# Performance work log

Hardware: AMD Instinct MI355X
Metric: run time of the kernel (lower is better)

Reference implementation:

```python
import jax, jax.numpy as jnp
import numpy as np

B, NPG, H, TD, NF, NL, A = 64, 20, 512, 256, 128, 6, 100
N = B * NPG
E = B * NPG * (NPG - 1)
ANG_LO, ANG_HI = 59.9, 120.1
LOG_MEANS = jnp.array([1.575442910194397, 1.7017393112182617, 1.9781638383865356], jnp.float32)
LOG_STDS = jnp.array([0.24437622725963593, 0.26526379585266113, 0.3535512685775757], jnp.float32)
TWO_PI = 2.0 * np.pi


def _logmap(x, y):
    z = TWO_PI * (y - x)
    return jnp.arctan2(jnp.sin(z), jnp.cos(z)) / TWO_PI


def _lattice_matrix(lengths, angles_deg):
    a = jnp.deg2rad(angles_deg)
    c, s = jnp.cos(a), jnp.sin(a)
    val = jnp.clip((c[:, 0] * c[:, 1] - c[:, 2]) / (s[:, 0] * s[:, 1]), -1.0, 1.0)
    gs = jnp.arccos(val)
    zero = jnp.zeros_like(lengths[:, 0])
    va = jnp.stack([lengths[:, 0] * s[:, 1], zero, lengths[:, 0] * c[:, 1]], 1)
    vb = jnp.stack([-lengths[:, 1] * s[:, 0] * jnp.cos(gs), lengths[:, 1] * s[:, 0] * jnp.sin(gs), lengths[:, 1] * c[:, 0]], 1)
    vc = jnp.stack([zero, zero, lengths[:, 2]], 1)
    return jnp.stack([va, vb, vc], 1)


def _ln(x, g, b, eps=1e-5):
    mu = jnp.mean(x, -1, keepdims=True)
    var = jnp.var(x, -1, keepdims=True)
    return (x - mu) * jax.lax.rsqrt(var + eps) * g + b


def setup_inputs() -> dict:
    key = jax.random.key(0)
    ks = jax.random.split(key, 24)
    # forward data
    t = jax.random.uniform(ks[0], (B, 1), jnp.float32)
    atom_types = jax.random.randint(ks[1], (N,), 1, A + 1, jnp.int32)
    frac_coords = jax.random.uniform(ks[2], (N, 3), jnp.float32)
    lattice_params = 0.5 * jax.random.normal(ks[3], (B, 6), jnp.float32)
    num_atoms = jnp.full((B,), NPG, jnp.int32)
    node2graph = jnp.repeat(jnp.arange(B, dtype=jnp.int32), NPG)
    # fully-connected edges per graph, no self edges (static structure)
    loc = np.arange(NPG)
    src_l, dst_l = np.meshgrid(loc, loc, indexing='ij')
    mask = src_l != dst_l
    src_l, dst_l = src_l[mask], dst_l[mask]  # (NPG*(NPG-1),)
    offs = (np.arange(B)[:, None] * NPG)
    src = (offs + src_l[None, :]).reshape(-1)
    dst = (offs + dst_l[None, :]).reshape(-1)
    edge_index = jnp.asarray(np.stack([src, dst]), jnp.int32)  # (2, E)
    edge2graph = node2graph[edge_index[0]]
    # parameters
    def w(k, shape, fan_in):
        return (jax.random.normal(k, shape, jnp.float32) / np.sqrt(fan_in)).astype(jnp.float32)
    EIN = 3 + 3 * H + 6 + NF * 2 * 3  # 2313
    p = {
        'W_node': w(ks[4], (A, H), A),
        'W_time': w(ks[5], (1, TD), 1),
        'W_latent': w(ks[6], (H + TD, H), H + TD),
        'ln_gamma': jnp.ones((NL, H), jnp.float32),
        'ln_beta': jnp.zeros((NL, H), jnp.float32),
        'We1': w(ks[7], (NL, EIN, H), EIN),
        'be1': jnp.zeros((NL, H), jnp.float32),
        'We2': w(ks[8], (NL, H, H), H),
        'be2': jnp.zeros((NL, H), jnp.float32),
        'Wn1': w(ks[9], (NL, 2 * H, H), 2 * H),
        'bn1': jnp.zeros((NL, H), jnp.float32),
        'Wn2': w(ks[10], (NL, H, H), H),
        'bn2': jnp.zeros((NL, H), jnp.float32),
        'W_numatom': w(ks[11], (NL, A, H), A),
        'fln_gamma': jnp.ones((H,), jnp.float32),
        'fln_beta': jnp.zeros((H,), jnp.float32),
        'W_coord': w(ks[12], (H, 3), H),
        'W_latout': w(ks[13], (2 * H, 6), 2 * H),
        'b_latout': jnp.zeros((6,), jnp.float32),
    }
    return dict(t=t, frac_coords=frac_coords, lattice_params=lattice_params,
                atom_types=atom_types, num_atoms=num_atoms, node2graph=node2graph,
                edge_index=edge_index, edge2graph=edge2graph, **p)


def reference(t, frac_coords, lattice_params, W_node, W_time, W_latent, ln_gamma, ln_beta,
              We1, be1, We2, be2, Wn1, bn1, Wn2, bn2, W_numatom, fln_gamma, fln_beta,
              W_coord, W_latout, b_latout, atom_types, num_atoms, node2graph, edge_index, edge2graph):
    n_nodes = frac_coords.shape[0]
    n_graphs = t.shape[0]
    src, dst = edge_index[0], edge_index[1]
    frac_diff = _logmap(frac_coords[src], frac_coords[dst])  # (E,3)

    atom_oh = jax.nn.one_hot(jnp.clip(atom_types - 1, 0), A, dtype=jnp.float32)
    h = atom_oh @ W_node
    temb = t @ W_time  # (B,TD)
    h = jnp.concatenate([h, temb[node2graph]], -1) @ W_latent

    lattice_flat = lattice_params  # 6-D in directly
    lengths = jnp.exp(lattice_params[:, :3] * LOG_STDS + LOG_MEANS)
    angles_deg = ANG_LO + (ANG_HI - ANG_LO) * jax.nn.sigmoid(lattice_params[:, 3:])
    Lmat = _lattice_matrix(lengths, angles_deg)  # (B,3,3)
    ltl = jnp.einsum('bij,bkj->bik', Lmat, Lmat)  # L @ L^T

    dots = jnp.einsum('eij,ej->ei', ltl[edge2graph], frac_diff)
    unit_dots = dots / (jnp.linalg.norm(dots, axis=-1, keepdims=True) + 1e-12)

    freqs = TWO_PI * jnp.arange(NF, dtype=jnp.float32)
    emb = (frac_diff[..., None] * freqs).reshape(-1, 3 * NF)
    femb = jnp.concatenate([jnp.sin(emb), jnp.cos(emb)], -1)  # (E, 768)

    na_oh = jax.nn.one_hot(num_atoms - 1, A, dtype=jnp.float32)  # (B,100)
    lat_e = lattice_flat[edge2graph]
    counts = jnp.maximum(jax.ops.segment_sum(jnp.ones_like(src, dtype=jnp.float32), src, num_segments=n_nodes), 1.0)[:, None]

    for l in range(NL):
        h_in = h
        hn = _ln(h_in, ln_gamma[l], ln_beta[l])
        na_emb = (na_oh @ W_numatom[l])[edge2graph]
        ef = jnp.concatenate([unit_dots, hn[src], hn[dst], lat_e, femb, na_emb], -1)
        e = jax.nn.silu(jax.nn.silu(ef @ We1[l] + be1[l]) @ We2[l] + be2[l])
        agg = jax.ops.segment_sum(e, src, num_segments=n_nodes) / counts
        out = jax.nn.silu(jax.nn.silu(jnp.concatenate([hn, agg], -1) @ Wn1[l] + bn1[l]) @ Wn2[l] + bn2[l])
        h = h_in + out

    h = _ln(h, fln_gamma, fln_beta)
    pos_v = h @ W_coord  # (N,3)
    sum_pool = jax.ops.segment_sum(h, node2graph, num_segments=n_graphs)
    mean_pool = sum_pool / num_atoms.astype(jnp.float32)[:, None]
    cell_v = jnp.concatenate([mean_pool, sum_pool], -1) @ W_latout + b_latout  # (B,6)
    return pos_v, cell_v
```

## Files before the change

### kernel.cpp

```cpp
#include <hip/hip_runtime.h>
#include <hip/hip_bf16.h>

typedef __hip_bfloat16 bf16;
typedef unsigned char u8;
typedef __attribute__((ext_vector_type(8))) __bf16 bf16x8;
typedef __attribute__((ext_vector_type(4))) float f32x4;

#define B_   64
#define NPG_ 20
#define H_   512
#define TD_  256
#define NF_  128
#define NL_  6
#define A_   100
#define N_   (B_ * NPG_)
#define E_   (B_ * NPG_ * (NPG_-1))
#define EIN_ 2313
#define KF_  832

__device__ __forceinline__ float bf2f(bf16 x) { return __bfloat162float(x); }
__device__ __forceinline__ bf16  f2bf(float x) { return __float2bfloat16(x); }
__device__ __forceinline__ float siluf(float x) { return x / (1.0f + expf(-x)); }
__device__ __forceinline__ float ldf(const void* p, size_t i, int isb) {
    return isb ? bf2f(((const bf16*)p)[i]) : ((const float*)p)[i];
}
__device__ __forceinline__ u8 f2f8(float f) {
    unsigned s = (__float_as_uint(f) >> 24) & 0x80;
    float a = fabsf(f);
    if (!(a == a)) return (u8)0x7F;
    if (a == 0.0f) return (u8)s;
    if (a >= 448.0f) return (u8)(s | 0x7E);
    int e; float m = frexpf(a, &e);
    int ef = e + 6;
    unsigned code;
    if (ef >= 1) {
        int mant = (int)rintf(m * 16.0f) - 8;
        if (mant == 8) { mant = 0; ef++; }
        if (ef > 15) return (u8)(s | 0x7E);
        code = ((unsigned)ef << 3) | (unsigned)mant;
    } else {
        int mant = (int)rintf(ldexpf(a, 9));
        code = (mant >= 8) ? (1u<<3) : (unsigned)mant;
    }
    return (u8)(s | code);
}
__device__ __forceinline__ void async_cp16(const void* src, void* dst) {
    __builtin_amdgcn_global_load_lds(
        (const __attribute__((address_space(1))) unsigned int*)src,
        (__attribute__((address_space(3))) unsigned int*)dst,
        16, 0, 0);
}

__global__ void detect_dtype(const unsigned int* __restrict__ tw, int* __restrict__ flag) {
    if (threadIdx.x != 0) return;
    int cnt = 0;
    for (int i = 0; i < 32; i++) {
        unsigned b1 = (tw[i] >> 8) & 0xFF;
        if (b1 >= 0x20 && b1 < 0x40) cnt++;
    }
    *flag = (cnt >= 16) ? 1 : 0;
}

__global__ void ws_sentinel(bf16* out) { if (threadIdx.x == 0) out[0] = f2bf(1000.0f); }

__global__ void prep_graph(const void* __restrict__ latp, float* __restrict__ ltl,
                           const int* __restrict__ flag) {
    int b = threadIdx.x;
    if (b >= B_) return;
    int isb = *flag;
    const float LM[3] = {1.575442910194397f, 1.7017393112182617f, 1.9781638383865356f};
    const float LS[3] = {0.24437622725963593f, 0.26526379585266113f, 0.3535512685775757f};
    float lp[6];
    for (int i = 0; i < 6; i++) lp[i] = ldf(latp, b*6 + i, isb);
    float len[3], c[3], s[3];
    for (int i = 0; i < 3; i++) len[i] = expf(lp[i] * LS[i] + LM[i]);
    for (int i = 0; i < 3; i++) {
        float sig = 1.0f / (1.0f + expf(-lp[3+i]));
        float deg = 59.9f + 60.2f * sig;
        float a = deg * 0.017453292519943295f;
        c[i] = cosf(a); s[i] = sinf(a);
    }
    float val = (c[0]*c[1] - c[2]) / (s[0]*s[1]);
    val = fminf(1.0f, fmaxf(-1.0f, val));
    float gs = acosf(val);
    float L[3][3];
    L[0][0] = len[0]*s[1]; L[0][1] = 0.0f;               L[0][2] = len[0]*c[1];
    L[1][0] = -len[1]*s[0]*cosf(gs); L[1][1] = len[1]*s[0]*sinf(gs); L[1][2] = len[1]*c[0];
    L[2][0] = 0.0f; L[2][1] = 0.0f; L[2][2] = len[2];
    for (int i = 0; i < 3; i++)
        for (int k = 0; k < 3; k++)
            ltl[b*9 + i*3 + k] = L[i][0]*L[k][0] + L[i][1]*L[k][1] + L[i][2]*L[k][2];
}

__global__ __launch_bounds__(512) void prep_q(const void* __restrict__ W_time,
                                              const void* __restrict__ W_latent,
                                              float* __restrict__ q,
                                              const int* __restrict__ flag) {
    int j = threadIdx.x;
    int isb = *flag;
    float s0 = 0.0f, s1 = 0.0f, s2 = 0.0f, s3 = 0.0f;
    for (int d = 0; d < TD_; d += 4) {
        s0 += ldf(W_time, d+0, isb) * ldf(W_latent, (size_t)(H_ + d+0)*H_ + j, isb);
        s1 += ldf(W_time, d+1, isb) * ldf(W_latent, (size_t)(H_ + d+1)*H_ + j, isb);
        s2 += ldf(W_time, d+2, isb) * ldf(W_latent, (size_t)(H_ + d+2)*H_ + j, isb);
        s3 += ldf(W_time, d+3, isb) * ldf(W_latent, (size_t)(H_ + d+3)*H_ + j, isb);
    }
    q[j] = (s0 + s1) + (s2 + s3);
}

__global__ __launch_bounds__(256) void pq_gather(const void* __restrict__ W_node,
                                                 const void* __restrict__ W_numatom,
                                                 bf16* __restrict__ PQa,
                                                 const int* __restrict__ flag) {
    int z = blockIdx.x, ch = blockIdx.y;
    int isb = *flag;
    int base = ch * 4096;
    for (int idx = base + threadIdx.x; idx < base + 4096; idx += 256) {
        int r = idx >> 9, c = idx & 511;
        float v = 0.0f;
        if (r < A_) {
            if (z == 0) v = ldf(W_node, (size_t)r*512 + c, isb);
            else        v = ldf(W_numatom, ((size_t)(z-1)*A_ + r)*512 + c, isb);
        }
        PQa[(size_t)z*65536 + idx] = f2bf(v);
    }
}

__global__ __launch_bounds__(256) void transpose_pq(const void* __restrict__ W_latent,
                                                    const void* __restrict__ We1,
                                                    bf16* __restrict__ PQbt,
                                                    const int* __restrict__ flag) {
    __shared__ bf16 tile[32][33];
    int z = blockIdx.z;
    int isb = *flag;
    const void* src = (z == 0) ? W_latent : We1;
    size_t off = (z == 0) ? 0 : ((size_t)(z-1)*EIN_ + 1801)*512;
    bf16* dst = PQbt + (size_t)z*512*512;
    int r0 = blockIdx.y * 32, c0 = blockIdx.x * 32;
    #pragma unroll
    for (int i = 0; i < 32; i += 8)
        tile[threadIdx.y + i][threadIdx.x] =
            f2bf(ldf(src, off + (size_t)(r0 + threadIdx.y + i)*512 + c0 + threadIdx.x, isb));
    __syncthreads();
    #pragma unroll
    for (int i = 0; i < 32; i += 8)
        dst[(size_t)(c0 + threadIdx.y + i)*512 + r0 + threadIdx.x] = tile[threadIdx.x][threadIdx.y + i];
}

__global__ __launch_bounds__(256) void transpose_layer(
    const void* __restrict__ We1p, const void* __restrict__ We2p,
    const void* __restrict__ Wn1p, const void* __restrict__ Wn2p, size_t l0, int allmode,
    bf16* __restrict__ WtAB, u8* __restrict__ Wtf8, bf16* __restrict__ Wte2,
    bf16* __restrict__ Wtn1, bf16* __restrict__ Wtn2,
    const int* __restrict__ flag) {
    __shared__ bf16 tile[32][33];
    int which = blockIdx.z % 6;
    size_t lz = blockIdx.z / 6;
    size_t l = l0 + lz, lw = allmode ? lz : 0;
    int isb = *flag;
    const void* src; size_t off; bf16* dst = nullptr; int R; int ldd;
    switch (which) {
        case 0:  src = We1p; off = (l*EIN_ + 3)*512;    dst = WtAB + lw*512*1024;            R = 512;  ldd = 512;  break;
        case 1:  src = We1p; off = (l*EIN_ + 515)*512;  dst = WtAB + lw*512*1024 + 512*512;  R = 512;  ldd = 512;  break;
        case 2:  src = We1p; off = (l*EIN_ + 1033)*512; R = 768; ldd = KF_; break;
        case 3:  src = We2p; off = l*512*512;           dst = Wte2 + lw*512*512;             R = 512;  ldd = 512;  break;
        case 4:  src = Wn1p; off = l*1024*512;          dst = Wtn1 + lw*512*1024;            R = 1024; ldd = 1024; break;
        default: src = Wn2p; off = l*512*512;           dst = Wtn2 + lw*512*512;             R = 512;  ldd = 512;  break;
    }
    int r0 = blockIdx.y * 32, c0 = blockIdx.x * 32;
    if (r0 >= R) return;
    #pragma unroll
    for (int i = 0; i < 32; i += 8)
        tile[threadIdx.y + i][threadIdx.x] =
            f2bf(ldf(src, off + (size_t)(r0 + threadIdx.y + i)*512 + c0 + threadIdx.x, isb));
    __syncthreads();
    if (which == 2) {
        u8* d8 = Wtf8 + lw*(size_t)512*KF_;
        #pragma unroll
        for (int i = 0; i < 32; i += 8)
            d8[(size_t)(c0 + threadIdx.y + i)*KF_ + r0 + threadIdx.x] =
                f2f8(bf2f(tile[threadIdx.x][threadIdx.y + i]));
    } else {
        #pragma unroll
        for (int i = 0; i < 32; i += 8)
            dst[(size_t)(c0 + threadIdx.y + i)*ldd + r0 + threadIdx.x] = tile[threadIdx.x][threadIdx.y + i];
    }
}

__global__ __launch_bounds__(512) void wtf_tail(const void* __restrict__ We1, size_t l0, int allmode,
                                                u8* __restrict__ Wtf8,
                                                const int* __restrict__ flag) {
    size_t lz = blockIdx.x;
    size_t l = l0 + lz, lw = allmode ? lz : 0;
    int n = threadIdx.x;
    int isb = *flag;
    const int rows[9] = {0, 1, 2, 1027, 1028, 1029, 1030, 1031, 1032};
    u8* d8 = Wtf8 + lw*(size_t)512*KF_;
    #pragma unroll
    for (int j = 0; j < 64; j++) {
        float v = (j < 9) ? ldf(We1, (l*EIN_ + rows[j])*512 + n, isb) : 0.0f;
        d8[(size_t)n*KF_ + 768 + j] = f2f8(v);
    }
}

__global__ __launch_bounds__(512) void cbias_prep(const bf16* __restrict__ PQc,
                                                  const void* __restrict__ be1,
                                                  const int* __restrict__ num_atoms,
                                                  float* __restrict__ cbias,
                                                  const int* __restrict__ flag) {
    int l = blockIdx.x, g = blockIdx.y, j = threadIdx.x;
    int isb = *flag;
    int na = num_atoms[g] - 1;
    float qv = (na >= 0 && na < A_) ? bf2f(PQc[(size_t)(1+l)*65536 + (size_t)na*512 + j]) : 0.0f;
    cbias[((size_t)l*B_ + g)*512 + j] = ldf(be1, l*512 + j, isb) + qv;
}

__global__ __launch_bounds__(512) void node_embed_fast(const bf16* __restrict__ P,
                                                       const float* __restrict__ q,
                                                       const void* __restrict__ t,
                                                       const int* __restrict__ atom_types,
                                                       const int* __restrict__ node2graph,
                                                       float* __restrict__ h,
                                                       const int* __restrict__ flag) {
    int i = blockIdx.x, j = threadIdx.x;
    int isb = *flag;
    int at = atom_types[i] - 1; if (at < 0) at = 0;
    float pv = (at < A_) ? bf2f(P[(size_t)at*512 + j]) : 0.0f;
    float tv = ldf(t, node2graph[i], isb);
    h[(size_t)i*H_ + j] = pv + tv * q[j];
}

__global__ __launch_bounds__(384) void edge_prep(const void* __restrict__ frac,
                                                 const int* __restrict__ edge_index,
                                                 const int* __restrict__ e2g,
                                                 const void* __restrict__ latp,
                                                 const float* __restrict__ ltl,
                                                 int* __restrict__ edat,
                                                 u8* __restrict__ femb8,
                                                 const int* __restrict__ flag) {
    const float TWO_PI_F = 6.283185307179586f;
    int e = blockIdx.x;
    int isb = *flag;
    int src = edge_index[e], dst = edge_index[E_ + e];
    int tid = threadIdx.x;
    int d = tid >> 7, k = tid & 127;
    float x = ldf(frac, src*3 + d, isb), y = ldf(frac, dst*3 + d, isb);
    float diff = y - x;
    float fd = diff - rintf(diff);
    float sv, cv;
    sincosf(fd * (TWO_PI_F * (float)k), &sv, &cv);
    femb8[(size_t)e*KF_ + d*NF_ + k]       = f2f8(sv);
    femb8[(size_t)e*KF_ + 384 + d*NF_ + k] = f2f8(cv);
    if (tid < 64) {
        int g = e2g[e];
        float v = 0.0f;
        if (tid < 3) {
            float f3[3];
            for (int dd = 0; dd < 3; dd++) {
                float df = ldf(frac, dst*3 + dd, isb) - ldf(frac, src*3 + dd, isb);
                f3[dd] = df - rintf(df);
            }
            float dots[3];
            for (int i = 0; i < 3; i++)
                dots[i] = ltl[g*9 + i*3 + 0]*f3[0] + ltl[g*9 + i*3 + 1]*f3[1] + ltl[g*9 + i*3 + 2]*f3[2];
            float nrm = sqrtf(dots[0]*dots[0] + dots[1]*dots[1] + dots[2]*dots[2]);
            v = dots[tid] / (nrm + 1e-12f);
        } else if (tid < 9) {
            v = ldf(latp, g*6 + tid - 3, isb);
        }
        femb8[(size_t)e*KF_ + 768 + tid] = f2f8(v);
        if (tid == 0) {
            edat[e*4 + 0] = src;
            edat[e*4 + 1] = dst;
            edat[e*4 + 2] = g;
            edat[e*4 + 3] = 0;
        }
    }
}

__device__ __forceinline__ float block_sum_256(float v, float* red) {
    for (int o = 32; o; o >>= 1) v += __shfl_down(v, o);
    int w = threadIdx.x >> 6, lane = threadIdx.x & 63;
    if (lane == 0) red[w] = v;
    __syncthreads();
    float s = red[0] + red[1] + red[2] + red[3];
    __syncthreads();
    return s;
}

__global__ __launch_bounds__(256) void ln_kernel(const float* __restrict__ x,
                                                 const void* __restrict__ gamma,
                                                 const void* __restrict__ beta, size_t goff,
                                                 bf16* __restrict__ cat,
                                                 const int* __restrict__ flag) {
    __shared__ float red[4];
    size_t n = blockIdx.x;
    int tid = threadIdx.x;
    int isb = *flag;
    const float* xr = x + n*H_;
    float v0 = xr[tid], v1 = xr[tid + 256];
    float mu = block_sum_256(v0 + v1, red) * (1.0f/512.0f);
    float d0 = v0 - mu, d1 = v1 - mu;
    float var = block_sum_256(d0*d0 + d1*d1, red) * (1.0f/512.0f);
    float rs = 1.0f / sqrtf(var + 1e-5f);
    cat[n*1024 + tid]       = f2bf(d0*rs*ldf(gamma, goff + tid, isb)       + ldf(beta, goff + tid, isb));
    cat[n*1024 + 256 + tid] = f2bf(d1*rs*ldf(gamma, goff + tid + 256, isb) + ldf(beta, goff + tid + 256, isb));
}

template<int EPI, int TM>
__global__ __launch_bounds__(256) void gemm_bt(
        const bf16* __restrict__ A, int lda,
        const bf16* __restrict__ Bt,
        const void* __restrict__ bias, size_t boff,
        bf16* __restrict__ Cb, float* __restrict__ Cf,
        int K, int N,
        size_t zsA, size_t zsB, size_t zsC,
        const int* __restrict__ flag) {
    constexpr int MT = TM / 32;
    __shared__ __align__(16) bf16 As[TM*64];
    __shared__ __align__(16) bf16 Bs[128*64];
    const int z = blockIdx.z;
    A  += (size_t)z * zsA;
    Bt += (size_t)z * zsB;
    const size_t coff = (size_t)z * zsC;
    const int tid = threadIdx.x;
    const int wave = tid >> 6, lane = tid & 63;
    const int lrow = lane & 15, lq = lane >> 4;
    const size_t m0 = (size_t)blockIdx.y * TM;
    const int n0 = blockIdx.x * 128;
    const int wm = (wave >> 1) * (TM/2), wn = (wave & 1) * 64;
    const int ar = lane >> 3;
    const int gk = (lane & 7) ^ ar;
    f32x4 acc[MT][4] = {};

    for (int k0 = 0; k0 < K; k0 += 64) {
        if (k0) __syncthreads();
        #pragma unroll
        for (int i = 0; i < TM/32; i++) {
            int R = wave*(TM/4) + i*8;
            async_cp16(A + (m0 + R + ar)*lda + k0 + gk*8, As + R*64);
        }
        #pragma unroll
        for (int i = 0; i < 4; i++) {
            int R = wave*32 + i*8;
            async_cp16(Bt + (size_t)(n0 + R + ar)*K + k0 + gk*8, Bs + R*64);
        }
        __syncthreads();
        #pragma unroll
        for (int kk = 0; kk < 2; kk++) {
            bf16x8 af[MT], bfr[4];
            #pragma unroll
            for (int mt = 0; mt < MT; mt++) {
                int r = wm + mt*16 + lrow;
                int p = (kk*4 + lq) ^ (r & 7);
                af[mt] = *(const bf16x8*)(As + r*64 + p*8);
            }
            #pragma unroll
            for (int nt = 0; nt < 4; nt++) {
                int r = wn + nt*16 + lrow;
                int p = (kk*4 + lq) ^ (r & 7);
                bfr[nt] = *(const bf16x8*)(Bs + r*64 + p*8);
            }
            #pragma unroll
            for (int mt = 0; mt < MT; mt++)
                #pragma unroll
                for (int nt = 0; nt < 4; nt++)
                    acc[mt][nt] = __builtin_amdgcn_mfma_f32_16x16x32_bf16(af[mt], bfr[nt], acc[mt][nt], 0, 0, 0);
        }
    }

    const int isb = bias ? *flag : 0;
    #pragma unroll
    for (int mt = 0; mt < MT; mt++)
        #pragma unroll
        for (int nt = 0; nt < 4; nt++) {
            int col = n0 + wn + nt*16 + lrow;
            float bv = bias ? ldf(bias, boff + col, isb) : 0.0f;
            #pragma unroll
            for (int r = 0; r < 4; r++) {
                size_t row = m0 + wm + mt*16 + lq*4 + r;
                float x = acc[mt][nt][r] + bv;
                if (EPI == 0)      Cb[coff + row*N + col] = f2bf(x);
                else if (EPI == 1) Cb[coff + row*N + col] = f2bf(siluf(x));
                else               Cf[coff + row*N + col] += siluf(x);
            }
        }
}

__global__ __launch_bounds__(256) void gemm_fp8_e1(
        const u8* __restrict__ A,
        const u8* __restrict__ Bt,
        const float* __restrict__ cbias_l,
        const bf16* __restrict__ hnAB,
        const int* __restrict__ edat,
        bf16* __restrict__ Cb) {
    __shared__ __align__(16) u8 As[64*64];
    __shared__ __align__(16) u8 Bs[128*64];
    const int tid = threadIdx.x;
    const int wave = tid >> 6, lane = tid & 63;
    const int lrow = lane & 15, lq = lane >> 4;
    const size_t m0 = (size_t)blockIdx.y * 64;
    const int n0 = blockIdx.x * 128;
    const int wm = (wave >> 1) * 32, wn = (wave & 1) * 64;
    const int ar = lane >> 2;
    const int ac = lane & 3;
    const int gk = ac ^ (ar & 3);
    f32x4 acc[2][4] = {};

    for (int k0 = 0; k0 < KF_; k0 += 64) {
        if (k0) __syncthreads();
        {
            int R = wave*16;
            async_cp16(A + (m0 + R + ar)*KF_ + k0 + gk*16, As + R*64);
        }
        #pragma unroll
        for (int i = 0; i < 2; i++) {
            int R = wave*32 + i*16;
            async_cp16(Bt + (size_t)(n0 + R + ar)*KF_ + k0 + gk*16, Bs + R*64);
        }
        __syncthreads();
        #pragma unroll
        for (int kk = 0; kk < 2; kk++) {
            long long af[2], bfr[4];
            #pragma unroll
            for (int mt = 0; mt < 2; mt++) {
                int r = wm + mt*16 + lrow;
                int p = (kk*2 + (lq >> 1)) ^ (r & 3);
                af[mt] = *(const long long*)(As + r*64 + p*16 + (lq & 1)*8);
            }
            #pragma unroll
            for (int nt = 0; nt < 4; nt++) {
                int r = wn + nt*16 + lrow;
                int p = (kk*2 + (lq >> 1)) ^ (r & 3);
                bfr[nt] = *(const long long*)(Bs + r*64 + p*16 + (lq & 1)*8);
            }
            #pragma unroll
            for (int mt = 0; mt < 2; mt++)
                #pragma unroll
                for (int nt = 0; nt < 4; nt++)
                    acc[mt][nt] = __builtin_amdgcn_mfma_f32_16x16x32_fp8_fp8(af[mt], bfr[nt], acc[mt][nt], 0, 0, 0);
        }
    }

    #pragma unroll
    for (int mt = 0; mt < 2; mt++) {
        #pragma unroll
        for (int r = 0; r < 4; r++) {
            size_t e = m0 + wm + mt*16 + lq*4 + r;
            const int4 q = *(const int4*)(edat + e*4);
            int se = q.x, de = q.y, g = q.z;
            #pragma unroll
            for (int nt = 0; nt < 4; nt++) {
                int col = n0 + wn + nt*16 + lrow;
                float x = acc[mt][nt][r]
                        + cbias_l[(size_t)g*512 + col]
                        + bf2f(hnAB[(size_t)se*1024 + col])
                        + bf2f(hnAB[(size_t)de*1024 + 512 + col]);
                Cb[e*512 + col] = f2bf(siluf(x));
            }
        }
    }
}

__global__ __launch_bounds__(256) void seg_mean(const bf16* __restrict__ e2,
                                                bf16* __restrict__ cat) {
    int n = blockIdx.x;
    #pragma unroll
    for (int jj = 0; jj < 2; jj++) {
        int j = threadIdx.x + jj*256;
        const bf16* base = e2 + (size_t)n*19*H_ + j;
        float s = 0.0f;
        #pragma unroll
        for (int i = 0; i < 19; i++) s += bf2f(base[(size_t)i*H_]);
        cat[(size_t)n*1024 + 512 + j] = f2bf(s / 19.0f);
    }
}

__global__ __launch_bounds__(256) void pos_out(const bf16* __restrict__ hln,
                                               const void* __restrict__ W_coord,
                                               void* __restrict__ out,
                                               const int* __restrict__ flag) {
    int wave = threadIdx.x >> 6, lane = threadIdx.x & 63;
    int n = blockIdx.x*4 + wave;
    int isb = *flag;
    float s0 = 0, s1 = 0, s2 = 0;
    for (int k = lane; k < H_; k += 64) {
        float hv = bf2f(hln[(size_t)n*1024 + k]);
        s0 += hv * ldf(W_coord, k*3 + 0, isb);
        s1 += hv * ldf(W_coord, k*3 + 1, isb);
        s2 += hv * ldf(W_coord, k*3 + 2, isb);
    }
    for (int o = 32; o; o >>= 1) {
        s0 += __shfl_down(s0, o); s1 += __shfl_down(s1, o); s2 += __shfl_down(s2, o);
    }
    if (lane == 0) {
        if (isb) { bf16* o = (bf16*)out;  o[n*3] = f2bf(s0); o[n*3+1] = f2bf(s1); o[n*3+2] = f2bf(s2); }
        else     { float* o = (float*)out; o[n*3] = s0; o[n*3+1] = s1; o[n*3+2] = s2; }
    }
}

__global__ __launch_bounds__(512) void cell_out(const bf16* __restrict__ hln,
                                                const void* __restrict__ W_latout,
                                                const void* __restrict__ b_latout,
                                                const int* __restrict__ num_atoms,
                                                void* __restrict__ out,
                                                const int* __restrict__ flag) {
    __shared__ float red[8*6];
    int b = blockIdx.x, j = threadIdx.x;
    int isb = *flag;
    float s = 0.0f;
    for (int i = 0; i < NPG_; i++) s += bf2f(hln[(size_t)(b*NPG_ + i)*1024 + j]);
    float m = s / (float)num_atoms[b];
    float p[6];
    #pragma unroll
    for (int c = 0; c < 6; c++)
        p[c] = m * ldf(W_latout, j*6 + c, isb) + s * ldf(W_latout, (512 + j)*6 + c, isb);
    int w = j >> 6, lane = j & 63;
    #pragma unroll
    for (int c = 0; c < 6; c++) {
        float v = p[c];
        for (int o = 32; o; o >>= 1) v += __shfl_down(v, o);
        if (lane == 0) red[w*6 + c] = v;
    }
    __syncthreads();
    if (j < 6) {
        float v = 0.0f;
        for (int w2 = 0; w2 < 8; w2++) v += red[w2*6 + j];
        float r = v + ldf(b_latout, j, isb);
        if (isb) ((bf16*)out)[N_*3 + b*6 + j] = f2bf(r);
        else     ((float*)out)[N_*3 + b*6 + j] = r;
    }
}

extern "C" void kernel_launch(void* const* d_in, const int* in_sizes, int n_in,
                              void* d_out, int out_size, void* d_ws, size_t ws_size,
                              hipStream_t stream) {
    const void* t          = d_in[0];
    const void* frac       = d_in[1];
    const void* latp       = d_in[2];
    const int*  atom_types = (const int*)d_in[3];
    const int*  num_atoms  = (const int*)d_in[4];
    const int*  node2graph = (const int*)d_in[5];
    const int*  edge_index = (const int*)d_in[6];
    const int*  e2g        = (const int*)d_in[7];
    const void* W_node     = d_in[8];
    const void* W_time     = d_in[9];
    const void* W_latent   = d_in[10];
    const void* ln_gamma   = d_in[11];
    const void* ln_beta    = d_in[12];
    const void* We1        = d_in[13];
    const void* be1        = d_in[14];
    const void* We2        = d_in[15];
    const void* be2        = d_in[16];
    const void* Wn1        = d_in[17];
    const void* bn1        = d_in[18];
    const void* Wn2        = d_in[19];
    const void* bn2        = d_in[20];
    const void* W_numatom  = d_in[21];
    const void* fln_gamma  = d_in[22];
    const void* fln_beta   = d_in[23];
    const void* W_coord    = d_in[24];
    const void* W_latout   = d_in[25];
    const void* b_latout   = d_in[26];

    const size_t fixed =
        256 + ((size_t)B_*9*4 + 255 & ~255ull) + 2048 + (size_t)N_*H_*4 + (size_t)E_*16
        + (size_t)N_*1024*2 + (size_t)E_*KF_ + (size_t)E_*H_*2*2 + (size_t)N_*1024*2
        + (size_t)N_*H_*2 + (size_t)7*128*512*2 + (size_t)NL_*B_*512*4 + 8192;
    const size_t perlayer_w = (size_t)512*1024*2 + (size_t)512*KF_ + (size_t)512*512*2
                            + (size_t)512*1024*2 + (size_t)512*512*2 + 2048;
    int allmode = (fixed + 6*perlayer_w <= ws_size) ? 1 : 0;
    size_t nw = allmode ? 6 : 1;

    char* p = (char*)d_ws;
    auto alloc = [&](size_t bytes) { char* r = p; p += (bytes + 255) & ~(size_t)255; return r; };
    int*   flag  = (int*)alloc(4);
    float* ltl   = (float*)alloc((size_t)B_*9*4);
    float* q     = (float*)alloc((size_t)H_*4);
    float* h     = (float*)alloc((size_t)N_*H_*4);
    int*   edat  = (int*)alloc((size_t)E_*4*4);
    bf16* hnAB  = (bf16*)alloc((size_t)N_*1024*2);
    u8*   femb8 = (u8*)alloc((size_t)E_*KF_);
    bf16* e1    = (bf16*)alloc((size_t)E_*H_*2);
    bf16* e2    = (bf16*)alloc((size_t)E_*H_*2);
    bf16* cat   = (bf16*)alloc((size_t)N_*1024*2);
    bf16* n1s   = (bf16*)alloc((size_t)N_*H_*2);
    bf16* PQc   = (bf16*)alloc((size_t)7*128*512*2);
    float* cbias = (float*)alloc((size_t)NL_*B_*512*4);
    bf16* WtAB  = (bf16*)alloc(nw*(size_t)512*1024*2);
    u8*   Wtf8  = (u8*)alloc(nw*(size_t)512*KF_);
    bf16* Wte2  = (bf16*)alloc(nw*(size_t)512*512*2);
    bf16* Wtn1  = (bf16*)alloc(nw*(size_t)512*1024*2);
    bf16* Wtn2  = (bf16*)alloc(nw*(size_t)512*512*2);
    bf16* PQa   = e1;
    bf16* PQbt  = e2;

    if ((size_t)(p - (char*)d_ws) > ws_size) {
        ws_sentinel<<<1, 64, 0, stream>>>((bf16*)d_out);
        return;
    }

    detect_dtype<<<1, 64, 0, stream>>>((const unsigned int*)t, flag);
    prep_graph<<<1, 64, 0, stream>>>(latp, ltl, flag);
    prep_q<<<1, 512, 0, stream>>>(W_time, W_latent, q, flag);
    pq_gather<<<dim3(7, 16), 256, 0, stream>>>(W_node, W_numatom, PQa, flag);
    transpose_pq<<<dim3(16, 16, 7), dim3(32, 8), 0, stream>>>(W_latent, We1, PQbt, flag);
    gemm_bt<0,128><<<dim3(4, 1, 7), 256, 0, stream>>>(
        PQa, 512, PQbt, nullptr, 0, PQc, nullptr, 512, 512,
        (size_t)128*512, (size_t)512*512, (size_t)128*512, flag);
    cbias_prep<<<dim3(NL_, B_), 512, 0, stream>>>(PQc, be1, num_atoms, cbias, flag);
    node_embed_fast<<<N_, 512, 0, stream>>>(PQc, q, t, atom_types, node2graph, h, flag);
    edge_prep<<<E_, 384, 0, stream>>>(frac, edge_index, e2g, latp, ltl, edat, femb8, flag);

    if (allmode) {
        transpose_layer<<<dim3(16, 32, 36), dim3(32, 8), 0, stream>>>(
            We1, We2, Wn1, Wn2, 0, 1, WtAB, Wtf8, Wte2, Wtn1, Wtn2, flag);
        wtf_tail<<<6, 512, 0, stream>>>(We1, 0, 1, Wtf8, flag);
    }

    for (size_t l = 0; l < NL_; l++) {
        size_t lw = allmode ? l : 0;
        bf16* WtABl = WtAB + lw*512*1024;
        u8*   Wtf8l = Wtf8 + lw*(size_t)512*KF_;
        bf16* Wte2l = Wte2 + lw*512*512;
        bf16* Wtn1l = Wtn1 + lw*512*1024;
        bf16* Wtn2l = Wtn2 + lw*512*512;
        if (!allmode) {
            transpose_layer<<<dim3(16, 32, 6), dim3(32, 8), 0, stream>>>(
                We1, We2, Wn1, Wn2, l, 0, WtAB, Wtf8, Wte2, Wtn1, Wtn2, flag);
            wtf_tail<<<1, 512, 0, stream>>>(We1, l, 0, Wtf8, flag);
        }
        ln_kernel<<<N_, 256, 0, stream>>>(h, ln_gamma, ln_beta, l*H_, cat, flag);
        gemm_bt<0,64><<<dim3(8, N_/64), 256, 0, stream>>>(
            cat, 1024, WtABl, nullptr, 0, hnAB, nullptr, 512, 1024, 0, 0, 0, flag);
        gemm_fp8_e1<<<dim3(4, E_/64), 256, 0, stream>>>(
            femb8, Wtf8l, cbias + l*B_*512, hnAB, edat, e1);
        gemm_bt<1,64><<<dim3(4, E_/64), 256, 0, stream>>>(
            e1, 512, Wte2l, be2, l*H_, e2, nullptr, 512, 512, 0, 0, 0, flag);
        seg_mean<<<N_, 256, 0, stream>>>(e2, cat);
        gemm_bt<1,64><<<dim3(4, N_/64), 256, 0, stream>>>(
            cat, 1024, Wtn1l, bn1, l*H_, n1s, nullptr, 1024, 512, 0, 0, 0, flag);
        gemm_bt<2,64><<<dim3(4, N_/64), 256, 0, stream>>>(
            n1s, 512, Wtn2l, bn2, l*H_, nullptr, h, 512, 512, 0, 0, 0, flag);
    }

    ln_kernel<<<N_, 256, 0, stream>>>(h, fln_gamma, fln_beta, 0, cat, flag);
    pos_out<<<N_/4, 256, 0, stream>>>(cat, W_coord, d_out, flag);
    cell_out<<<B_, 512, 0, stream>>>(cat, W_latout, b_latout, num_atoms, d_out, flag);
}
```

Baseline: 1.057 ms.

## Run the second edge GEMM in FP8 and widen the FP8 K-tile to 128

```diff
diff --git a/kernel.cpp b/kernel.cpp
--- a/kernel.cpp
+++ b/kernel.cpp
@@ -3,8 +3,10 @@
 
 typedef __hip_bfloat16 bf16;
 typedef unsigned char u8;
+typedef long long i64;
 typedef __attribute__((ext_vector_type(8))) __bf16 bf16x8;
 typedef __attribute__((ext_vector_type(4))) float f32x4;
+typedef __attribute__((ext_vector_type(2))) i64 i64x2;
 
 #define B_   64
 #define NPG_ 20
@@ -16,13 +18,16 @@
 #define N_   (B_ * NPG_)
 #define E_   (B_ * NPG_ * (NPG_-1))
 #define EIN_ 2313
-#define KF_  832
+#define KF8_ 896
 
 __device__ __forceinline__ float bf2f(bf16 x) { return __bfloat162float(x); }
 __device__ __forceinline__ bf16  f2bf(float x) { return __float2bfloat16(x); }
 __device__ __forceinline__ float siluf(float x) { return x / (1.0f + expf(-x)); }
 __device__ __forceinline__ float ldf(const void* p, size_t i, int isb) {
     return isb ? bf2f(((const bf16*)p)[i]) : ((const float*)p)[i];
+}
+__device__ __forceinline__ int perm_k(int o) {
+    return (o & ~127) | (((o >> 3) & 3) << 5) | (((o >> 5) & 3) << 3) | (o & 7);
 }
 __device__ __forceinline__ u8 f2f8(float f) {
     unsigned s = (__float_as_uint(f) >> 24) & 0x80;
@@ -150,7 +155,7 @@
 __global__ __launch_bounds__(256) void transpose_layer(
     const void* __restrict__ We1p, const void* __restrict__ We2p,
     const void* __restrict__ Wn1p, const void* __restrict__ Wn2p, size_t l0, int allmode,
-    bf16* __restrict__ WtAB, u8* __restrict__ Wtf8, bf16* __restrict__ Wte2,
+    bf16* __restrict__ WtAB, u8* __restrict__ Wtf8, u8* __restrict__ Wte28,
     bf16* __restrict__ Wtn1, bf16* __restrict__ Wtn2,
     const int* __restrict__ flag) {
     __shared__ bf16 tile[32][33];
@@ -158,14 +163,14 @@
     size_t lz = blockIdx.z / 6;
     size_t l = l0 + lz, lw = allmode ? lz : 0;
     int isb = *flag;
-    const void* src; size_t off; bf16* dst = nullptr; int R; int ldd;
+    const void* src; size_t off; bf16* dst = nullptr; u8* d8 = nullptr; int R; int ldd;
     switch (which) {
         case 0:  src = We1p; off = (l*EIN_ + 3)*512;    dst = WtAB + lw*512*1024;            R = 512;  ldd = 512;  break;
         case 1:  src = We1p; off = (l*EIN_ + 515)*512;  dst = WtAB + lw*512*1024 + 512*512;  R = 512;  ldd = 512;  break;
-        case 2:  src = We1p; off = (l*EIN_ + 1033)*512; R = 768; ldd = KF_; break;
-        case 3:  src = We2p; off = l*512*512;           dst = Wte2 + lw*512*512;             R = 512;  ldd = 512;  break;
+        case 2:  src = We1p; off = (l*EIN_ + 1033)*512; d8 = Wtf8 + lw*(size_t)512*KF8_;     R = 768;  ldd = KF8_; break;
+        case 3:  src = We2p; off = l*512*512;           d8 = Wte28 + lw*(size_t)512*512;     R = 512;  ldd = 512;  break;
         case 4:  src = Wn1p; off = l*1024*512;          dst = Wtn1 + lw*512*1024;            R = 1024; ldd = 1024; break;
-        default: src = Wn2p; off = l*512*512;           dst = Wtn2 + lw*512*512;             R = 512;  ldd = 512;  break;
+        default: src = Wn2p; off = l*512*512;           dst = Wtn2 + lw*512*512;             R = 512;  ldd = 512; break;
     }
     int r0 = blockIdx.y * 32, c0 = blockIdx.x * 32;
     if (r0 >= R) return;
@@ -174,11 +179,11 @@
         tile[threadIdx.y + i][threadIdx.x] =
             f2bf(ldf(src, off + (size_t)(r0 + threadIdx.y + i)*512 + c0 + threadIdx.x, isb));
     __syncthreads();
-    if (which == 2) {
-        u8* d8 = Wtf8 + lw*(size_t)512*KF_;
+    if (which == 2 || which == 3) {
+        int kp = perm_k(r0 + threadIdx.x);
         #pragma unroll
         for (int i = 0; i < 32; i += 8)
-            d8[(size_t)(c0 + threadIdx.y + i)*KF_ + r0 + threadIdx.x] =
+            d8[(size_t)(c0 + threadIdx.y + i)*ldd + kp] =
                 f2f8(bf2f(tile[threadIdx.x][threadIdx.y + i]));
     } else {
         #pragma unroll
@@ -195,11 +200,11 @@
     int n = threadIdx.x;
     int isb = *flag;
     const int rows[9] = {0, 1, 2, 1027, 1028, 1029, 1030, 1031, 1032};
-    u8* d8 = Wtf8 + lw*(size_t)512*KF_;
-    #pragma unroll
-    for (int j = 0; j < 64; j++) {
+    u8* d8 = Wtf8 + lw*(size_t)512*KF8_;
+    #pragma unroll
+    for (int j = 0; j < 128; j++) {
         float v = (j < 9) ? ldf(We1, (l*EIN_ + rows[j])*512 + n, isb) : 0.0f;
-        d8[(size_t)n*KF_ + 768 + j] = f2f8(v);
+        d8[(size_t)n*KF8_ + perm_k(768 + j)] = f2f8(v);
     }
 }
 
@@ -249,9 +254,9 @@
     float fd = diff - rintf(diff);
     float sv, cv;
     sincosf(fd * (TWO_PI_F * (float)k), &sv, &cv);
-    femb8[(size_t)e*KF_ + d*NF_ + k]       = f2f8(sv);
-    femb8[(size_t)e*KF_ + 384 + d*NF_ + k] = f2f8(cv);
-    if (tid < 64) {
+    femb8[(size_t)e*KF8_ + perm_k(d*NF_ + k)]       = f2f8(sv);
+    femb8[(size_t)e*KF8_ + perm_k(384 + d*NF_ + k)] = f2f8(cv);
+    if (tid < 128) {
         int g = e2g[e];
         float v = 0.0f;
         if (tid < 3) {
@@ -268,7 +273,7 @@
         } else if (tid < 9) {
             v = ldf(latp, g*6 + tid - 3, isb);
         }
-        femb8[(size_t)e*KF_ + 768 + tid] = f2f8(v);
+        femb8[(size_t)e*KF8_ + perm_k(768 + tid)] = f2f8(v);
         if (tid == 0) {
             edat[e*4 + 0] = src;
             edat[e*4 + 1] = dst;
@@ -387,78 +392,101 @@
         }
 }
 
-__global__ __launch_bounds__(256) void gemm_fp8_e1(
+template<int EPI>
+__global__ __launch_bounds__(256) void gemm_fp8(
         const u8* __restrict__ A,
         const u8* __restrict__ Bt,
+        int K,
         const float* __restrict__ cbias_l,
         const bf16* __restrict__ hnAB,
         const int* __restrict__ edat,
-        bf16* __restrict__ Cb) {
-    __shared__ __align__(16) u8 As[64*64];
-    __shared__ __align__(16) u8 Bs[128*64];
+        u8* __restrict__ C8,
+        const void* __restrict__ bias, size_t boff,
+        bf16* __restrict__ Cb,
+        const int* __restrict__ flag) {
+    __shared__ __align__(16) u8 As[64*128];
+    __shared__ __align__(16) u8 Bs[128*128];
     const int tid = threadIdx.x;
     const int wave = tid >> 6, lane = tid & 63;
     const int lrow = lane & 15, lq = lane >> 4;
     const size_t m0 = (size_t)blockIdx.y * 64;
     const int n0 = blockIdx.x * 128;
     const int wm = (wave >> 1) * 32, wn = (wave & 1) * 64;
-    const int ar = lane >> 2;
-    const int ac = lane & 3;
-    const int gk = ac ^ (ar & 3);
+    const int ar = lane >> 3;
+    const int gk = (lane & 7) ^ ar;
     f32x4 acc[2][4] = {};
 
-    for (int k0 = 0; k0 < KF_; k0 += 64) {
+    for (int k0 = 0; k0 < K; k0 += 128) {
         if (k0) __syncthreads();
-        {
-            int R = wave*16;
-            async_cp16(A + (m0 + R + ar)*KF_ + k0 + gk*16, As + R*64);
-        }
         #pragma unroll
         for (int i = 0; i < 2; i++) {
-            int R = wave*32 + i*16;
-            async_cp16(Bt + (size_t)(n0 + R + ar)*KF_ + k0 + gk*16, Bs + R*64);
+            int R = wave*16 + i*8;
+            async_cp16(A + (size_t)(m0 + R + ar)*K + k0 + gk*16, As + R*128);
+        }
+        #pragma unroll
+        for (int i = 0; i < 4; i++) {
+            int R = wave*32 + i*8;
+            async_cp16(Bt + (size_t)(n0 + R + ar)*K + k0 + gk*16, Bs + R*128);
         }
         __syncthreads();
         #pragma unroll
-        for (int kk = 0; kk < 2; kk++) {
-            long long af[2], bfr[4];
+        for (int kp = 0; kp < 2; kp++) {
+            i64x2 af[2], bfr[4];
             #pragma unroll
             for (int mt = 0; mt < 2; mt++) {
                 int r = wm + mt*16 + lrow;
-                int p = (kk*2 + (lq >> 1)) ^ (r & 3);
-                af[mt] = *(const long long*)(As + r*64 + p*16 + (lq & 1)*8);
+                int q = (lq*2 + kp) ^ (r & 7);
+                af[mt] = *(const i64x2*)(As + r*128 + q*16);
             }
             #pragma unroll
             for (int nt = 0; nt < 4; nt++) {
                 int r = wn + nt*16 + lrow;
-                int p = (kk*2 + (lq >> 1)) ^ (r & 3);
-                bfr[nt] = *(const long long*)(Bs + r*64 + p*16 + (lq & 1)*8);
+                int q = (lq*2 + kp) ^ (r & 7);
+                bfr[nt] = *(const i64x2*)(Bs + r*128 + q*16);
             }
             #pragma unroll
             for (int mt = 0; mt < 2; mt++)
                 #pragma unroll
-                for (int nt = 0; nt < 4; nt++)
-                    acc[mt][nt] = __builtin_amdgcn_mfma_f32_16x16x32_fp8_fp8(af[mt], bfr[nt], acc[mt][nt], 0, 0, 0);
-        }
-    }
-
-    #pragma unroll
-    for (int mt = 0; mt < 2; mt++) {
-        #pragma unroll
-        for (int r = 0; r < 4; r++) {
-            size_t e = m0 + wm + mt*16 + lq*4 + r;
-            const int4 q = *(const int4*)(edat + e*4);
-            int se = q.x, de = q.y, g = q.z;
+                for (int nt = 0; nt < 4; nt++) {
+                    acc[mt][nt] = __builtin_amdgcn_mfma_f32_16x16x32_fp8_fp8(af[mt].x, bfr[nt].x, acc[mt][nt], 0, 0, 0);
+                    acc[mt][nt] = __builtin_amdgcn_mfma_f32_16x16x32_fp8_fp8(af[mt].y, bfr[nt].y, acc[mt][nt], 0, 0, 0);
+                }
+        }
+    }
+
+    if constexpr (EPI == 3) {
+        #pragma unroll
+        for (int mt = 0; mt < 2; mt++) {
+            #pragma unroll
+            for (int r = 0; r < 4; r++) {
+                size_t e = m0 + wm + mt*16 + lq*4 + r;
+                const int4 q = *(const int4*)(edat + e*4);
+                int se = q.x, de = q.y, g = q.z;
+                #pragma unroll
+                for (int nt = 0; nt < 4; nt++) {
+                    int col = n0 + wn + nt*16 + lrow;
+                    float x = acc[mt][nt][r]
+                            + cbias_l[(size_t)g*512 + col]
+                            + bf2f(hnAB[(size_t)se*1024 + col])
+                            + bf2f(hnAB[(size_t)de*1024 + 512 + col]);
+                    C8[e*512 + perm_k(col)] = f2f8(siluf(x));
+                }
+            }
+        }
+    } else {
+        const int isb = *flag;
+        #pragma unroll
+        for (int mt = 0; mt < 2; mt++)
             #pragma unroll
             for (int nt = 0; nt < 4; nt++) {
                 int col = n0 + wn + nt*16 + lrow;
-                float x = acc[mt][nt][r]
-                        + cbias_l[(size_t)g*512 + col]
-                        + bf2f(hnAB[(size_t)se*1024 + col])
-                        + bf2f(hnAB[(size_t)de*1024 + 512 + col]);
-                Cb[e*512 + col] = f2bf(siluf(x));
-            }
-        }
+                float bv = ldf(bias, boff + col, isb);
+                #pragma unroll
+                for (int r = 0; r < 4; r++) {
+                    size_t row = m0 + wm + mt*16 + lq*4 + r;
+                    Cb[row*512 + col] = f2bf(siluf(acc[mt][nt][r] + bv));
+                }
+            }
     }
 }
 
@@ -563,12 +591,14 @@
     const void* W_latout   = d_in[25];
     const void* b_latout   = d_in[26];
 
+    auto AL = [](size_t b) { return (b + 255) & ~(size_t)255; };
     const size_t fixed =
-        256 + ((size_t)B_*9*4 + 255 & ~255ull) + 2048 + (size_t)N_*H_*4 + (size_t)E_*16
-        + (size_t)N_*1024*2 + (size_t)E_*KF_ + (size_t)E_*H_*2*2 + (size_t)N_*1024*2
-        + (size_t)N_*H_*2 + (size_t)7*128*512*2 + (size_t)NL_*B_*512*4 + 8192;
-    const size_t perlayer_w = (size_t)512*1024*2 + (size_t)512*KF_ + (size_t)512*512*2
-                            + (size_t)512*1024*2 + (size_t)512*512*2 + 2048;
+        AL(4) + AL((size_t)B_*9*4) + AL((size_t)H_*4) + AL((size_t)N_*H_*4)
+      + AL((size_t)E_*4*4) + AL((size_t)N_*1024*2) + AL((size_t)E_*KF8_)
+      + AL((size_t)E_*512) + AL((size_t)E_*H_*2) + AL((size_t)N_*1024*2)
+      + AL((size_t)N_*H_*2) + AL((size_t)7*128*512*2) + AL((size_t)NL_*B_*512*4);
+    const size_t perlayer_w = AL((size_t)512*1024*2) + AL((size_t)512*KF8_)
+                            + AL((size_t)512*512) + AL((size_t)512*1024*2) + AL((size_t)512*512*2);
     int allmode = (fixed + 6*perlayer_w <= ws_size) ? 1 : 0;
     size_t nw = allmode ? 6 : 1;
 
@@ -580,19 +610,19 @@
     float* h     = (float*)alloc((size_t)N_*H_*4);
     int*   edat  = (int*)alloc((size_t)E_*4*4);
     bf16* hnAB  = (bf16*)alloc((size_t)N_*1024*2);
-    u8*   femb8 = (u8*)alloc((size_t)E_*KF_);
-    bf16* e1    = (bf16*)alloc((size_t)E_*H_*2);
+    u8*   femb8 = (u8*)alloc((size_t)E_*KF8_);
+    u8*   e18   = (u8*)alloc((size_t)E_*512);
     bf16* e2    = (bf16*)alloc((size_t)E_*H_*2);
     bf16* cat   = (bf16*)alloc((size_t)N_*1024*2);
     bf16* n1s   = (bf16*)alloc((size_t)N_*H_*2);
     bf16* PQc   = (bf16*)alloc((size_t)7*128*512*2);
     float* cbias = (float*)alloc((size_t)NL_*B_*512*4);
     bf16* WtAB  = (bf16*)alloc(nw*(size_t)512*1024*2);
-    u8*   Wtf8  = (u8*)alloc(nw*(size_t)512*KF_);
-    bf16* Wte2  = (bf16*)alloc(nw*(size_t)512*512*2);
+    u8*   Wtf8  = (u8*)alloc(nw*(size_t)512*KF8_);
+    u8*   Wte28 = (u8*)alloc(nw*(size_t)512*512);
     bf16* Wtn1  = (bf16*)alloc(nw*(size_t)512*1024*2);
     bf16* Wtn2  = (bf16*)alloc(nw*(size_t)512*512*2);
-    bf16* PQa   = e1;
+    bf16* PQa   = (bf16*)e18;
     bf16* PQbt  = e2;
 
     if ((size_t)(p - (char*)d_ws) > ws_size) {
@@ -614,29 +644,29 @@
 
     if (allmode) {
         transpose_layer<<<dim3(16, 32, 36), dim3(32, 8), 0, stream>>>(
-            We1, We2, Wn1, Wn2, 0, 1, WtAB, Wtf8, Wte2, Wtn1, Wtn2, flag);
+            We1, We2, Wn1, Wn2, 0, 1, WtAB, Wtf8, Wte28, Wtn1, Wtn2, flag);
         wtf_tail<<<6, 512, 0, stream>>>(We1, 0, 1, Wtf8, flag);
     }
 
     for (size_t l = 0; l < NL_; l++) {
         size_t lw = allmode ? l : 0;
         bf16* WtABl = WtAB + lw*512*1024;
-        u8*   Wtf8l = Wtf8 + lw*(size_t)512*KF_;
-        bf16* Wte2l = Wte2 + lw*512*512;
+        u8*   Wtf8l = Wtf8 + lw*(size_t)512*KF8_;
+        u8*   Wte28l = Wte28 + lw*(size_t)512*512;
         bf16* Wtn1l = Wtn1 + lw*512*1024;
         bf16* Wtn2l = Wtn2 + lw*512*512;
         if (!allmode) {
             transpose_layer<<<dim3(16, 32, 6), dim3(32, 8), 0, stream>>>(
-                We1, We2, Wn1, Wn2, l, 0, WtAB, Wtf8, Wte2, Wtn1, Wtn2, flag);
+                We1, We2, Wn1, Wn2, l, 0, WtAB, Wtf8, Wte28, Wtn1, Wtn2, flag);
             wtf_tail<<<1, 512, 0, stream>>>(We1, l, 0, Wtf8, flag);
         }
         ln_kernel<<<N_, 256, 0, stream>>>(h, ln_gamma, ln_beta, l*H_, cat, flag);
         gemm_bt<0,64><<<dim3(8, N_/64), 256, 0, stream>>>(
             cat, 1024, WtABl, nullptr, 0, hnAB, nullptr, 512, 1024, 0, 0, 0, flag);
-        gemm_fp8_e1<<<dim3(4, E_/64), 256, 0, stream>>>(
-            femb8, Wtf8l, cbias + l*B_*512, hnAB, edat, e1);
-        gemm_bt<1,64><<<dim3(4, E_/64), 256, 0, stream>>>(
-            e1, 512, Wte2l, be2, l*H_, e2, nullptr, 512, 512, 0, 0, 0, flag);
+        gemm_fp8<3><<<dim3(4, E_/64), 256, 0, stream>>>(
+            femb8, Wtf8l, KF8_, cbias + l*B_*512, hnAB, edat, e18, nullptr, 0, nullptr, flag);
+        gemm_fp8<1><<<dim3(4, E_/64), 256, 0, stream>>>(
+            e18, Wte28l, 512, nullptr, nullptr, nullptr, nullptr, be2, l*H_, e2, flag);
         seg_mean<<<N_, 256, 0, stream>>>(e2, cat);
         gemm_bt<1,64><<<dim3(4, N_/64), 256, 0, stream>>>(
             cat, 1024, Wtn1l, bn1, l*H_, n1s, nullptr, 1024, 512, 0, 0, 0, flag);
```

New measurement: 1.110 ms. +5.1%, slower.
